# Optimization experiments

Measured on AMD Instinct MI355X. Metric: run time of the kernel, lower is better.

The kernel has to match this reference:

```python
import jax, jax.numpy as jnp
import numpy as np

N, E, G = 50000, 400000, 2048
H, C = 4, 64            # heads, hidden per head
IN, ED, TASKS = 29, 6, 12
HC = H * C


def setup_inputs() -> dict:
    key = jax.random.key(0)
    ks = jax.random.split(key, 20)
    s = 0.1
    f32 = jnp.float32
    inp = {
        'x': jax.random.normal(ks[0], (N, IN), f32),
        'edge_index': jax.random.randint(ks[1], (2, E), 0, N),
        'edge_attr': jax.random.normal(ks[2], (E, ED), f32),
        'batch': jnp.sort(jax.random.randint(ks[3], (N,), 0, G)),
        # layer 1 (in=29 -> H*C=256)
        'W1': jax.random.normal(ks[4], (IN, HC), f32) * s,
        'as1': jax.random.normal(ks[5], (1, H, C), f32) * s,
        'ad1': jax.random.normal(ks[6], (1, H, C), f32) * s,
        'We1': jax.random.normal(ks[7], (ED, HC), f32) * s,
        'ae1': jax.random.normal(ks[8], (1, H, C), f32) * s,
        'b1': jnp.zeros((HC,), f32),
        # layer 2 (in=256 -> 256)
        'W2': jax.random.normal(ks[9], (HC, HC), f32) * s,
        'as2': jax.random.normal(ks[10], (1, H, C), f32) * s,
        'ad2': jax.random.normal(ks[11], (1, H, C), f32) * s,
        'We2': jax.random.normal(ks[12], (ED, HC), f32) * s,
        'ae2': jax.random.normal(ks[13], (1, H, C), f32) * s,
        'b2': jnp.zeros((HC,), f32),
        # readout linear (256 -> 12)
        'Wl': jax.random.normal(ks[14], (HC, TASKS), f32) * s,
        'bl': jnp.zeros((TASKS,), f32),
    }
    return inp


def _gat_conv(x, src, dst, eattr, W, a_src, a_dst, We, a_e, b):
    """PyG GATConv, concat=True, leaky_relu slope 0.2, self-loops already appended."""
    h = (x @ W).reshape(N, H, C)                      # [N,H,C]
    al_s = jnp.sum(h * a_src, axis=-1)                # [N,H]
    al_d = jnp.sum(h * a_dst, axis=-1)                # [N,H]
    he = (eattr @ We).reshape(-1, H, C)               # [Etot,H,C]
    al_e = jnp.sum(he * a_e, axis=-1)                 # [Etot,H]
    alpha = al_s[src] + al_d[dst] + al_e              # [Etot,H]
    alpha = jax.nn.leaky_relu(alpha, negative_slope=0.2)
    # segment softmax over incoming edges of each dst node
    amax = jax.ops.segment_max(alpha, dst, num_segments=N)
    ex = jnp.exp(alpha - amax[dst])
    denom = jax.ops.segment_sum(ex, dst, num_segments=N)
    alpha = ex / (denom[dst] + 1e-16)
    msg = h[src] * alpha[:, :, None]                  # [Etot,H,C]
    out = jax.ops.segment_sum(msg, dst, num_segments=N)
    return out.reshape(N, HC) + b


def reference(x, edge_index, edge_attr, batch,
              W1, as1, ad1, We1, ae1, b1,
              W2, as2, ad2, We2, ae2, b2, Wl, bl):
    # add self-loops with edge_attr fill = mean over existing edges (PyG default)
    loop = jnp.arange(N)
    src = jnp.concatenate([edge_index[0], loop])
    dst = jnp.concatenate([edge_index[1], loop])
    mean_e = jnp.mean(edge_attr, axis=0, keepdims=True)
    eattr = jnp.concatenate([edge_attr, jnp.broadcast_to(mean_e, (N, ED))], axis=0)

    h = _gat_conv(x, src, dst, eattr, W1, as1, ad1, We1, ae1, b1)
    h = jax.nn.relu(h)
    h = _gat_conv(h, src, dst, eattr, W2, as2, ad2, We2, ae2, b2)
    h = jax.nn.relu(h)

    # global mean pool over graphs
    sums = jax.ops.segment_sum(h, batch, num_segments=G)      # [G,HC]
    cnt = jax.ops.segment_sum(jnp.ones((N,), h.dtype), batch, num_segments=G)
    pooled = sums / jnp.maximum(cnt, 1.0)[:, None]
    return pooled @ Wl + bl
```

## Files before the change

kernel.cpp:

```cpp
#include <hip/hip_runtime.h>
#include <math.h>

static constexpr int NN = 50000;
static constexpr int EE = 400000;
static constexpr int GG = 2048;
static constexpr int TASKS = 12;

typedef __attribute__((ext_vector_type(8))) short short8;
typedef __attribute__((ext_vector_type(4))) float floatx4;

__device__ __forceinline__ unsigned short f2bf(float f) {
  unsigned u = __float_as_uint(f);
  u = u + 0x7fffu + ((u >> 16) & 1u);
  return (unsigned short)(u >> 16);
}
__device__ __forceinline__ float bflo(unsigned u) { return __uint_as_float(u << 16); }
__device__ __forceinline__ float bfhi(unsigned u) { return __uint_as_float(u & 0xffff0000u); }

static constexpr int NBDEG = (EE + 255) / 256;
static constexpr int NBMEAN = 256;
static constexpr int NBX = (NN * 32 + 255) / 256;
static constexpr int NW1 = 32;
static constexpr int NW2 = 256;
__global__ void k_pre(const int* __restrict__ dst, const float* __restrict__ ea,
                      const float* __restrict__ x, const float* __restrict__ W1,
                      const float* __restrict__ W2, int* __restrict__ deg,
                      float* __restrict__ msum, unsigned short* __restrict__ xb,
                      unsigned short* __restrict__ w1t, unsigned short* __restrict__ w2t) {
  const int b = blockIdx.x;
  const int t = threadIdx.x;
  if (b < NBDEG) {
    int e = b * 256 + t;
    if (e < EE) atomicAdd(&deg[dst[e]], 1);
  } else if (b < NBDEG + NBMEAN) {
    float s[6] = {0, 0, 0, 0, 0, 0};
    for (int e = (b - NBDEG) * 256 + t; e < EE; e += NBMEAN * 256) {
#pragma unroll
      for (int d = 0; d < 6; d++) s[d] += ea[(size_t)e * 6 + d];
    }
    __shared__ float ls[6];
    if (t < 6) ls[t] = 0.f;
    __syncthreads();
#pragma unroll
    for (int d = 0; d < 6; d++) atomicAdd(&ls[d], s[d]);
    __syncthreads();
    if (t < 6) atomicAdd(&msum[t], ls[t]);
  } else if (b < NBDEG + NBMEAN + NBX) {
    int i = (b - NBDEG - NBMEAN) * 256 + t;
    if (i < NN * 32) {
      int n = i >> 5, k = i & 31;
      xb[i] = (k < 29) ? f2bf(x[(size_t)n * 29 + k]) : (unsigned short)0;
    }
  } else if (b < NBDEG + NBMEAN + NBX + NW1) {
    int i = (b - NBDEG - NBMEAN - NBX) * 256 + t;
    int n = i >> 5, k = i & 31;
    w1t[i] = (k < 29) ? f2bf(W1[(size_t)k * 256 + n]) : (unsigned short)0;
  } else {
    int i = (b - NBDEG - NBMEAN - NBX - NW1) * 256 + t;
    int n = i >> 8, k = i & 255;
    w2t[i] = f2bf(W2[(size_t)k * 256 + n]);
  }
}

__global__ void k_scan1(const int* __restrict__ deg, int* __restrict__ rowptr, int* __restrict__ bsums) {
  __shared__ int sh[256];
  int i = blockIdx.x * 256 + threadIdx.x;
  int v = (i < NN) ? deg[i] : 0;
  sh[threadIdx.x] = v;
  __syncthreads();
  for (int off = 1; off < 256; off <<= 1) {
    int t = (threadIdx.x >= off) ? sh[threadIdx.x - off] : 0;
    __syncthreads();
    sh[threadIdx.x] += t;
    __syncthreads();
  }
  if (i < NN) rowptr[i] = sh[threadIdx.x] - v;
  if (threadIdx.x == 255) bsums[blockIdx.x] = sh[255];
}

__global__ void k_scan23(int* __restrict__ rowptr, const int* __restrict__ bsums, int nb) {
  __shared__ int sh[256];
  const int t = threadIdx.x;
  sh[t] = (t < nb) ? bsums[t] : 0;
  __syncthreads();
  for (int off = 1; off < 256; off <<= 1) {
    int tv = (t >= off) ? sh[t - off] : 0;
    __syncthreads();
    sh[t] += tv;
    __syncthreads();
  }
  const int add = (blockIdx.x == 0) ? 0 : sh[blockIdx.x - 1];
  int i = blockIdx.x * 256 + t;
  if (i < NN) rowptr[i] += add;
  if (i == 0) rowptr[NN] = EE;
}

__global__ void k_scatparams(const int* __restrict__ ei, const int* __restrict__ rowptr,
                             int* __restrict__ cursor, int* __restrict__ csrc,
                             int* __restrict__ eslot, const float* __restrict__ We1,
                             const float* __restrict__ ae1, const float* __restrict__ We2,
                             const float* __restrict__ ae2, const float* __restrict__ msum,
                             float* __restrict__ p1, float* __restrict__ p2) {
  const int b = blockIdx.x;
  const int t = threadIdx.x;
  if (b < NBDEG) {
    int e = b * 256 + t;
    if (e >= EE) return;
    int s = ei[e];
    int d = ei[EE + e];
    int p = atomicAdd(&cursor[d], 1);
    int slot = rowptr[d] + p;
    csrc[slot] = s;
    eslot[e] = slot;
  } else {
    const int layer = b - NBDEG;
    const float* We = layer ? We2 : We1;
    const float* ae = layer ? ae2 : ae1;
    float* params = layer ? p2 : p1;
    __shared__ float vsh[24];
    if (t < 24) {
      int d = t >> 2, h = t & 3;
      float s = 0.f;
      for (int c = 0; c < 64; c++) s += We[d * 256 + h * 64 + c] * ae[h * 64 + c];
      vsh[t] = s;
      params[t] = s;
    }
    __syncthreads();
    if (t < 4) {
      float s = 0.f;
      const float invE = 1.0f / (float)EE;
#pragma unroll
      for (int d = 0; d < 6; d++) s += (msum[d] * invE) * vsh[d * 4 + t];
      params[24 + t] = s;
    }
  }
}

__global__ __launch_bounds__(256) void k_gemm_mfma(
    const unsigned short* __restrict__ A, const unsigned short* __restrict__ Bt,
    const float* __restrict__ a_s, const float* __restrict__ a_d,
    unsigned short* __restrict__ Y, float* __restrict__ als, float* __restrict__ ald,
    int M, int Kp) {
  constexpr int AP = 40;
  __shared__ unsigned short As[64 * AP];
  __shared__ unsigned short Bs[256 * AP];
  const int tid = threadIdx.x;
  const int lane = tid & 63;
  const int w = tid >> 6;
  const int l15 = lane & 15;
  const int quad = lane >> 4;
  const int row0 = blockIdx.x * 64;

  floatx4 acc[4][4];
#pragma unroll
  for (int i = 0; i < 4; i++)
#pragma unroll
    for (int j = 0; j < 4; j++) acc[i][j] = {0.f, 0.f, 0.f, 0.f};

  const int ar = tid >> 2;
  const int ac = tid & 3;

  for (int k0 = 0; k0 < Kp; k0 += 32) {
    {
      int row = row0 + ar;
      if (row >= M) row = M - 1;
      *(short8*)&As[ar * AP + ac * 8] = *(const short8*)(A + (size_t)row * Kp + k0 + ac * 8);
    }
    {
      const unsigned short* bp = Bt + (size_t)tid * Kp + k0;
#pragma unroll
      for (int c = 0; c < 4; c++) *(short8*)&Bs[tid * AP + c * 8] = *(const short8*)(bp + c * 8);
    }
    __syncthreads();
    short8 af[4], bfr[4];
#pragma unroll
    for (int i = 0; i < 4; i++) af[i] = *(const short8*)&As[(i * 16 + l15) * AP + quad * 8];
#pragma unroll
    for (int j = 0; j < 4; j++) bfr[j] = *(const short8*)&Bs[(w * 64 + j * 16 + l15) * AP + quad * 8];
#pragma unroll
    for (int i = 0; i < 4; i++)
#pragma unroll
      for (int j = 0; j < 4; j++)
        acc[i][j] = __builtin_amdgcn_mfma_f32_16x16x32_bf16(af[i], bfr[j], acc[i][j], 0, 0, 0);
    __syncthreads();
  }
  float asc[4], adc[4];
#pragma unroll
  for (int j = 0; j < 4; j++) {
    asc[j] = a_s[w * 64 + j * 16 + l15];
    adc[j] = a_d[w * 64 + j * 16 + l15];
  }
#pragma unroll
  for (int i = 0; i < 4; i++) {
#pragma unroll
    for (int r = 0; r < 4; r++) {
      const int row = row0 + i * 16 + quad * 4 + r;
      unsigned ub[4];
      float hv[4];
#pragma unroll
      for (int j = 0; j < 4; j++) {
        ub[j] = f2bf(acc[i][j][r]);
        hv[j] = __uint_as_float(ub[j] << 16);
      }
      if (row < M) {
#pragma unroll
        for (int j = 0; j < 4; j++) Y[(size_t)row * 256 + w * 64 + j * 16 + l15] = (unsigned short)ub[j];
      }
      float ps = hv[0] * asc[0] + hv[1] * asc[1] + hv[2] * asc[2] + hv[3] * asc[3];
      float pd = hv[0] * adc[0] + hv[1] * adc[1] + hv[2] * adc[2] + hv[3] * adc[3];
#pragma unroll
      for (int off = 1; off < 16; off <<= 1) {
        ps += __shfl_xor(ps, off, 64);
        pd += __shfl_xor(pd, off, 64);
      }
      if (l15 == 0 && row < M) {
        als[row * 4 + w] = ps;
        ald[row * 4 + w] = pd;
      }
    }
  }
}

__device__ __forceinline__ float leaky02(float x) { return x > 0.f ? x : 0.2f * x; }

__global__ void k_edge(const int* __restrict__ ei, const float* __restrict__ ea,
                       const float* __restrict__ als, const float* __restrict__ ald,
                       const int* __restrict__ eslot, const float* __restrict__ params,
                       float* __restrict__ exa) {
  int e = blockIdx.x * blockDim.x + threadIdx.x;
  if (e >= EE) return;
  int src = ei[e], dst = ei[EE + e];
  float4 s4 = *(const float4*)(als + (size_t)src * 4);
  float4 d4 = *(const float4*)(ald + (size_t)dst * 4);
  float ed[6];
#pragma unroll
  for (int d = 0; d < 6; d++) ed[d] = ea[(size_t)e * 6 + d];
  float sl[4] = {s4.x + d4.x, s4.y + d4.y, s4.z + d4.z, s4.w + d4.w};
  float out[4];
#pragma unroll
  for (int h = 0; h < 4; h++) {
    float x = sl[h];
#pragma unroll
    for (int d = 0; d < 6; d++) x += ed[d] * params[d * 4 + h];
    out[h] = __expf(leaky02(x));
  }
  *(float4*)(exa + (size_t)eslot[e] * 4) = make_float4(out[0], out[1], out[2], out[3]);
}

__global__ __launch_bounds__(256) void k_agg(
    const unsigned short* __restrict__ hinb, const float* __restrict__ als,
    const float* __restrict__ ald, const int* __restrict__ rowptr, const int* __restrict__ csrc,
    const float* __restrict__ exa, const float* __restrict__ params, const float* __restrict__ bias,
    unsigned short* __restrict__ houtb) {
  const int lane = threadIdx.x & 63;
  const int n = blockIdx.x * 4 + (threadIdx.x >> 6);
  if (n >= NN) return;
  const int half = lane >> 5;
  const int sl = lane & 31;
  const int head = sl >> 3;

  float acc[8];
  float ssum;
  {
    float slg = leaky02(als[n * 4 + head] + ald[n * 4 + head] + params[24 + head]);
    float exs = __expf(slg);
    float wgt = (half == 0) ? exs : 0.f;
    ssum = wgt;
    uint4 uv = *(const uint4*)(hinb + (size_t)n * 256 + sl * 8);
    acc[0] = bflo(uv.x) * wgt;
    acc[1] = bfhi(uv.x) * wgt;
    acc[2] = bflo(uv.y) * wgt;
    acc[3] = bfhi(uv.y) * wgt;
    acc[4] = bflo(uv.z) * wgt;
    acc[5] = bfhi(uv.z) * wgt;
    acc[6] = bflo(uv.w) * wgt;
    acc[7] = bfhi(uv.w) * wgt;
  }
  const int end = rowptr[n + 1];
  int s = rowptr[n] + half;
  int sn = 0;
  float ex = 0.f;
  if (s < end) {
    sn = csrc[s];
    ex = exa[(size_t)s * 4 + head];
  }
  while (s < end) {
    const int sc = sn;
    const float exc = ex;
    const int s2 = s + 2;
    if (s2 < end) {
      sn = csrc[s2];
      ex = exa[(size_t)s2 * 4 + head];
    }
    uint4 uv = *(const uint4*)(hinb + (size_t)sc * 256 + sl * 8);
    acc[0] += bflo(uv.x) * exc;
    acc[1] += bfhi(uv.x) * exc;
    acc[2] += bflo(uv.y) * exc;
    acc[3] += bfhi(uv.y) * exc;
    acc[4] += bflo(uv.z) * exc;
    acc[5] += bfhi(uv.z) * exc;
    acc[6] += bflo(uv.w) * exc;
    acc[7] += bfhi(uv.w) * exc;
    ssum += exc;
    s = s2;
  }
#pragma unroll
  for (int j = 0; j < 8; j++) acc[j] += __shfl_xor(acc[j], 32, 64);
  ssum += __shfl_xor(ssum, 32, 64);
  if (half == 0) {
    const float inv = 1.f / (ssum + 1e-16f);
    float4 b0 = *(const float4*)(bias + sl * 8);
    float4 b1 = *(const float4*)(bias + sl * 8 + 4);
    const float bb[8] = {b0.x, b0.y, b0.z, b0.w, b1.x, b1.y, b1.z, b1.w};
    uint p[4];
#pragma unroll
    for (int j = 0; j < 4; j++) {
      float e0 = fmaxf(acc[2 * j] * inv + bb[2 * j], 0.f);
      float e1 = fmaxf(acc[2 * j + 1] * inv + bb[2 * j + 1], 0.f);
      p[j] = (uint)f2bf(e0) | ((uint)f2bf(e1) << 16);
    }
    *(uint4*)(houtb + (size_t)n * 256 + sl * 8) = make_uint4(p[0], p[1], p[2], p[3]);
  }
}

__global__ __launch_bounds__(256) void k_pool(const unsigned short* __restrict__ hb,
                                              const int* __restrict__ batch,
                                              const float* __restrict__ Wl,
                                              const float* __restrict__ bl,
                                              float* __restrict__ out) {
  int g = blockIdx.x;
  int t = threadIdx.x;
  int lo = 0, hi = NN;
  while (lo < hi) {
    int mid = (lo + hi) >> 1;
    if (batch[mid] < g) lo = mid + 1; else hi = mid;
  }
  int start = lo;
  hi = NN;
  while (lo < hi) {
    int mid = (lo + hi) >> 1;
    if (batch[mid] < g + 1) lo = mid + 1; else hi = mid;
  }
  int end = lo;
  __shared__ float sp[256];
  if (t < 128) {
    float s0 = 0.f, s1 = 0.f;
    for (int n2 = start; n2 < end; n2++) {
      uint u = ((const uint*)(hb + (size_t)n2 * 256))[t];
      s0 += bflo(u);
      s1 += bfhi(u);
    }
    float invc = 1.f / fmaxf((float)(end - start), 1.f);
    sp[2 * t] = s0 * invc;
    sp[2 * t + 1] = s1 * invc;
  }
  __syncthreads();
  if (t < TASKS) {
    float o = bl[t];
    for (int c = 0; c < 256; c++) o += sp[c] * Wl[c * 12 + t];
    out[(size_t)g * 12 + t] = o;
  }
}

extern "C" void kernel_launch(void* const* d_in, const int* in_sizes, int n_in,
                              void* d_out, int out_size, void* d_ws, size_t ws_size,
                              hipStream_t stream) {
  const float* x = (const float*)d_in[0];
  const int* ei = (const int*)d_in[1];
  const float* ea = (const float*)d_in[2];
  const int* batch = (const int*)d_in[3];
  const float* W1 = (const float*)d_in[4];
  const float* as1 = (const float*)d_in[5];
  const float* ad1 = (const float*)d_in[6];
  const float* We1 = (const float*)d_in[7];
  const float* ae1 = (const float*)d_in[8];
  const float* b1 = (const float*)d_in[9];
  const float* W2 = (const float*)d_in[10];
  const float* as2 = (const float*)d_in[11];
  const float* ad2 = (const float*)d_in[12];
  const float* We2 = (const float*)d_in[13];
  const float* ae2 = (const float*)d_in[14];
  const float* b2 = (const float*)d_in[15];
  const float* Wl = (const float*)d_in[16];
  const float* bl = (const float*)d_in[17];
  float* out = (float*)d_out;

  char* ws = (char*)d_ws;
  size_t off = 0;
  auto take = [&](size_t bytes) -> char* {
    char* p = ws + off;
    off = (off + bytes + 255) & ~(size_t)255;
    return p;
  };
  float* msum = (float*)take(8 * 4);
  int* deg = (int*)take((size_t)NN * 4);
  int* cursor = (int*)take((size_t)NN * 4);
  size_t zero_end = off;
  int* rowptr = (int*)take((size_t)(NN + 1) * 4);
  int* bsums = (int*)take(256 * 4);
  int* csrc = (int*)take((size_t)EE * 4);
  int* eslot = (int*)take((size_t)EE * 4);
  float* exa = (float*)take((size_t)EE * 4 * 4);
  float* p1 = (float*)take(32 * 4);
  float* p2 = (float*)take(32 * 4);
  float* als = (float*)take((size_t)NN * 4 * 4);
  float* ald = (float*)take((size_t)NN * 4 * 4);
  unsigned short* hb = (unsigned short*)take((size_t)NN * 256 * 2);
  unsigned short* ab = (unsigned short*)take((size_t)NN * 256 * 2);
  unsigned short* xb = (unsigned short*)take((size_t)NN * 32 * 2);
  unsigned short* w1t = (unsigned short*)take((size_t)256 * 32 * 2);
  unsigned short* w2t = (unsigned short*)take((size_t)256 * 256 * 2);
  (void)ws_size;

  hipMemsetAsync(ws, 0, zero_end, stream);

  const int nbN = (NN + 255) / 256;
  const int nbE = (EE + 255) / 256;

  k_pre<<<NBDEG + NBMEAN + NBX + NW1 + NW2, 256, 0, stream>>>(ei + EE, ea, x, W1, W2,
                                                              deg, msum, xb, w1t, w2t);
  k_scan1<<<nbN, 256, 0, stream>>>(deg, rowptr, bsums);
  k_scan23<<<nbN, 256, 0, stream>>>(rowptr, bsums, nbN);
  k_scatparams<<<NBDEG + 2, 256, 0, stream>>>(ei, rowptr, cursor, csrc, eslot,
                                              We1, ae1, We2, ae2, msum, p1, p2);

  const int gb = (NN + 63) / 64;

  k_gemm_mfma<<<gb, 256, 0, stream>>>(xb, w1t, as1, ad1, hb, als, ald, NN, 32);
  k_edge<<<nbE, 256, 0, stream>>>(ei, ea, als, ald, eslot, p1, exa);
  k_agg<<<NN / 4, 256, 0, stream>>>(hb, als, ald, rowptr, csrc, exa, p1, b1, ab);

  k_gemm_mfma<<<gb, 256, 0, stream>>>(ab, w2t, as2, ad2, hb, als, ald, NN, 256);
  k_edge<<<nbE, 256, 0, stream>>>(ei, ea, als, ald, eslot, p2, exa);
  k_agg<<<NN / 4, 256, 0, stream>>>(hb, als, ald, rowptr, csrc, exa, p2, b2, ab);

  k_pool<<<GG, 256, 0, stream>>>(ab, batch, Wl, bl, out);
}
```

Measured before the change: 325.1 us.

## Drop LDS staging in MFMA GEMM, load fragments directly, widen row tile

The GEMM kernel no longer stages A and B tiles through shared memory with barriers. Each lane now loads its MFMA fragments straight from global memory through per-row pointers, and each block covers 128 rows instead of 64 so every B fragment feeds twice as many MFMAs. The x-to-bf16 conversion also writes 8 elements per thread as one vector store. The trade is that the four waves reload A redundantly from global memory or cache, register pressure rises from the larger accumulator array, and the grid has fewer blocks.

```diff
diff --git a/kernel.cpp b/kernel.cpp
--- a/kernel.cpp
+++ b/kernel.cpp
@@ -19,7 +19,7 @@
 
 static constexpr int NBDEG = (EE + 255) / 256;
 static constexpr int NBMEAN = 256;
-static constexpr int NBX = (NN * 32 + 255) / 256;
+static constexpr int NBX = (NN * 4 + 255) / 256;
 static constexpr int NW1 = 32;
 static constexpr int NW2 = 256;
 __global__ void k_pre(const int* __restrict__ dst, const float* __restrict__ ea,
@@ -47,9 +47,15 @@
     if (t < 6) atomicAdd(&msum[t], ls[t]);
   } else if (b < NBDEG + NBMEAN + NBX) {
     int i = (b - NBDEG - NBMEAN) * 256 + t;
-    if (i < NN * 32) {
-      int n = i >> 5, k = i & 31;
-      xb[i] = (k < 29) ? f2bf(x[(size_t)n * 29 + k]) : (unsigned short)0;
+    if (i < NN * 4) {
+      int n = i >> 2, seg = i & 3;
+      unsigned short v[8];
+#pragma unroll
+      for (int j = 0; j < 8; j++) {
+        int k = seg * 8 + j;
+        v[j] = (k < 29) ? f2bf(x[(size_t)n * 29 + k]) : (unsigned short)0;
+      }
+      *(short8*)(xb + (size_t)n * 32 + seg * 8) = *(short8*)v;
     }
   } else if (b < NBDEG + NBMEAN + NBX + NW1) {
     int i = (b - NBDEG - NBMEAN - NBX) * 256 + t;
@@ -141,48 +147,45 @@
     const float* __restrict__ a_s, const float* __restrict__ a_d,
     unsigned short* __restrict__ Y, float* __restrict__ als, float* __restrict__ ald,
     int M, int Kp) {
-  constexpr int AP = 40;
-  __shared__ unsigned short As[64 * AP];
-  __shared__ unsigned short Bs[256 * AP];
   const int tid = threadIdx.x;
   const int lane = tid & 63;
   const int w = tid >> 6;
   const int l15 = lane & 15;
   const int quad = lane >> 4;
-  const int row0 = blockIdx.x * 64;
-
-  floatx4 acc[4][4];
-#pragma unroll
-  for (int i = 0; i < 4; i++)
+  const int row0 = blockIdx.x * 128;
+
+  floatx4 acc[8][4];
+#pragma unroll
+  for (int i = 0; i < 8; i++)
 #pragma unroll
     for (int j = 0; j < 4; j++) acc[i][j] = {0.f, 0.f, 0.f, 0.f};
 
-  const int ar = tid >> 2;
-  const int ac = tid & 3;
+  const unsigned short* pa[8];
+  const unsigned short* pb[4];
+#pragma unroll
+  for (int i = 0; i < 8; i++) {
+    int r = row0 + i * 16 + l15;
+    if (r >= M) r = M - 1;
+    pa[i] = A + (size_t)r * Kp + quad * 8;
+  }
+#pragma unroll
+  for (int j = 0; j < 4; j++) pb[j] = Bt + (size_t)(w * 64 + j * 16 + l15) * Kp + quad * 8;
 
   for (int k0 = 0; k0 < Kp; k0 += 32) {
-    {
-      int row = row0 + ar;
-      if (row >= M) row = M - 1;
-      *(short8*)&As[ar * AP + ac * 8] = *(const short8*)(A + (size_t)row * Kp + k0 + ac * 8);
-    }
-    {
-      const unsigned short* bp = Bt + (size_t)tid * Kp + k0;
-#pragma unroll
-      for (int c = 0; c < 4; c++) *(short8*)&Bs[tid * AP + c * 8] = *(const short8*)(bp + c * 8);
-    }
-    __syncthreads();
-    short8 af[4], bfr[4];
-#pragma unroll
-    for (int i = 0; i < 4; i++) af[i] = *(const short8*)&As[(i * 16 + l15) * AP + quad * 8];
-#pragma unroll
-    for (int j = 0; j < 4; j++) bfr[j] = *(const short8*)&Bs[(w * 64 + j * 16 + l15) * AP + quad * 8];
-#pragma unroll
-    for (int i = 0; i < 4; i++)
+    short8 af[8], bfr[4];
+#pragma unroll
+    for (int i = 0; i < 8; i++) af[i] = *(const short8*)pa[i];
+#pragma unroll
+    for (int j = 0; j < 4; j++) bfr[j] = *(const short8*)pb[j];
+#pragma unroll
+    for (int i = 0; i < 8; i++) pa[i] += 32;
+#pragma unroll
+    for (int j = 0; j < 4; j++) pb[j] += 32;
+#pragma unroll
+    for (int i = 0; i < 8; i++)
 #pragma unroll
       for (int j = 0; j < 4; j++)
         acc[i][j] = __builtin_amdgcn_mfma_f32_16x16x32_bf16(af[i], bfr[j], acc[i][j], 0, 0, 0);
-    __syncthreads();
   }
   float asc[4], adc[4];
 #pragma unroll
@@ -191,7 +194,7 @@
     adc[j] = a_d[w * 64 + j * 16 + l15];
   }
 #pragma unroll
-  for (int i = 0; i < 4; i++) {
+  for (int i = 0; i < 8; i++) {
 #pragma unroll
     for (int r = 0; r < 4; r++) {
       const int row = row0 + i * 16 + quad * 4 + r;
@@ -424,7 +427,7 @@
   k_scatparams<<<NBDEG + 2, 256, 0, stream>>>(ei, rowptr, cursor, csrc, eslot,
                                               We1, ae1, We2, ae2, msum, p1, p2);
 
-  const int gb = (NN + 63) / 64;
+  const int gb = (NN + 127) / 128;
 
   k_gemm_mfma<<<gb, 256, 0, stream>>>(xb, w1t, as1, ad1, hb, als, ald, NN, 32);
   k_edge<<<nbE, 256, 0, stream>>>(ei, ea, als, ald, eslot, p1, exa);
```

Result: slower. 342.0 us (+5.2%).
